# Performance work log

Measured on AMD Instinct MI355X. Metric: run time of the kernel, lower is better.

## Reference

```python
import jax, jax.numpy as jnp
import numpy as np

N = 400_000
D = 128          # voxel grid extent per axis
IN_CH = 64
OUT_CH = 64
BOUND = 2.0


def _build_neighbor_map(rng):
    # unique voxel coordinates in a D^3 grid
    flat = rng.choice(D ** 3, size=N, replace=False)
    lut = np.full(D ** 3, N, dtype=np.int32)   # sentinel N = no point
    lut[flat] = np.arange(N, dtype=np.int32)
    coords = np.stack(np.unravel_index(flat, (D, D, D)), axis=1).astype(np.int64)  # [N,3]
    offs = np.array([[i, j, k] for i in (-1, 0, 1) for j in (-1, 0, 1) for k in (-1, 0, 1)],
                    dtype=np.int64)  # [27,3]
    nbr = np.empty((27, N), dtype=np.int32)
    for k in range(27):
        nc = coords + offs[k]
        valid = np.all((nc >= 0) & (nc < D), axis=1)
        ncc = np.clip(nc, 0, D - 1)
        fl = (ncc[:, 0] * D + ncc[:, 1]) * D + ncc[:, 2]
        nbr[k] = np.where(valid, lut[fl], N)
    return jnp.asarray(nbr)


def setup_inputs() -> dict:
    key = jax.random.key(0)
    k1, k2, k3, k4 = jax.random.split(key, 4)
    rng = np.random.default_rng(0)
    nbr = _build_neighbor_map(rng)
    return {
        "x_feat": jax.random.normal(k1, (N, IN_CH), jnp.float32),
        "y_feat": jax.random.normal(k2, (N, IN_CH), jnp.float32),
        "w1": jax.random.normal(k3, (27, 2 * IN_CH, IN_CH), jnp.float32) * 0.05,
        "b1": jnp.zeros((IN_CH,), jnp.float32),
        "w2": jax.random.normal(k4, (27, IN_CH, OUT_CH), jnp.float32) * 0.05,
        "b2": jnp.zeros((OUT_CH,), jnp.float32),
        "nbr": nbr,
    }


def _sparse_conv(feats, w, b, nbr):
    # feats: [N, Cin]; w: [27, Cin, Cout]; nbr: [27, N] with sentinel N -> zero feature
    fpad = jnp.concatenate([feats, jnp.zeros((1, feats.shape[1]), feats.dtype)], axis=0)

    def step(acc, wk_nk):
        wk, nk = wk_nk
        return acc + fpad[nk] @ wk, None

    acc0 = jnp.zeros((feats.shape[0], w.shape[2]), feats.dtype)
    out, _ = jax.lax.scan(step, acc0, (w, nbr))
    return out + b


def reference(x_feat, y_feat, w1, b1, w2, b2, nbr):
    # ME.cat((x, y)): concat features on shared coordinate map
    feats = jnp.concatenate([x_feat, y_feat], axis=1)            # [N, 2*in_ch]
    h = _sparse_conv(feats, w1, b1, nbr)                         # ConvBlock 1
    h = jax.nn.relu(h)                                           # act='relu'
    h = _sparse_conv(h, w2, b2, nbr)                             # ConvBlock 2 (act=None)
    return jnp.clip(h, -BOUND, BOUND)                            # BoundFunction forward
```

## Files before the change

kernel.cpp:

```cpp
#include <hip/hip_runtime.h>
#include <stdint.h>


#define NPTS 400000
#define TAPS 27

typedef __attribute__((ext_vector_type(8))) _Float16 f16x8;
typedef __attribute__((ext_vector_type(4))) float f32x4;

#define MFMA16(a, b, c) __builtin_amdgcn_mfma_f32_16x16x32_f16(a, b, c, 0, 0, 0)

#define H16_BYTES ((size_t)(NPTS + 1) * 128)
#define W1T_SZ    ((size_t)TAPS * 64 * 128 * 2)
#define W2T_SZ    ((size_t)TAPS * 64 * 64 * 2)
#define W1T_OFF   (H16_BYTES)
#define W2T_OFF   (W1T_OFF + W1T_SZ)
#define XY16_OFF  (W2T_OFF + W2T_SZ)

__device__ inline void gload_lds16(const void* g, void* l) {
    __builtin_amdgcn_global_load_lds((const __attribute__((address_space(1))) void*)g,
                                     (__attribute__((address_space(3))) void*)l, 16, 0, 0);
}

__global__ __launch_bounds__(256) void prep_weights(
    const float* __restrict__ w1, const float* __restrict__ w2,
    _Float16* __restrict__ w1t, _Float16* __restrict__ w2t,
    _Float16* __restrict__ h16)
{
    const int gid = blockIdx.x * 256 + threadIdx.x;
    const int n1 = TAPS * 64 * 128;
    const int n2 = TAPS * 64 * 64;
    if (gid < n1) {
        const int tap = gid >> 13;
        const int q  = (gid & 8191) << 1;
        const int sb = q ^ (((q >> 8) & 15) << 4);
        const int col = sb >> 8, k = (sb & 255) >> 1;
        w1t[gid] = (_Float16)w1[((size_t)tap * 128 + k) * 64 + col];
    } else if (gid < n1 + n2) {
        const int g = gid - n1;
        const int tap = g >> 12;
        const int q  = (g & 4095) << 1;
        const int sb = q ^ (((q >> 7) & 7) << 4);
        const int col = sb >> 7, k = (sb & 127) >> 1;
        w2t[g] = (_Float16)w2[((size_t)tap * 64 + k) * 64 + col];
    } else if (gid < n1 + n2 + 64) {
        h16[(size_t)NPTS * 64 + (gid - n1 - n2)] = (_Float16)0.f;
    }
}

__global__ __launch_bounds__(256) void prep_xy16(
    const float* __restrict__ x, const float* __restrict__ y,
    _Float16* __restrict__ xy16)
{
    const int gid = blockIdx.x * 256 + threadIdx.x;
    if (gid >= (NPTS + 1) * 16) return;
    const int p = gid >> 4, seg = gid & 15;
    f32x4 v0 = {0.f, 0.f, 0.f, 0.f}, v1 = {0.f, 0.f, 0.f, 0.f};
    if (p < NPTS) {
        const float* s = (seg < 8) ? (x + (size_t)p * 64 + seg * 8)
                                   : (y + (size_t)p * 64 + (seg - 8) * 8);
        v0 = *(const f32x4*)s; v1 = *(const f32x4*)(s + 4);
    }
    _Float16 h[8];
#pragma unroll
    for (int j = 0; j < 4; ++j) { h[j] = (_Float16)v0[j]; h[4 + j] = (_Float16)v1[j]; }
    *(f16x8*)&xy16[(size_t)p * 128 + seg * 8] = *(f16x8*)h;
}

__global__ __launch_bounds__(256, 4) void conv1_kernel(
    const _Float16* __restrict__ xy16,
    const _Float16* __restrict__ w1t,
    const float* __restrict__ b1, const int* __restrict__ nbr,
    _Float16* __restrict__ h16)
{
    __shared__ char wsh[16384];

    const int tid = threadIdx.x;
    const int wv = tid >> 6, ln = tid & 63;
    const int g4 = ln >> 4, c = ln & 15;
    const int base = blockIdx.x * 128 + wv * 32;

    f32x4 acc[2][4];
    {
        float bv[4];
#pragma unroll
        for (int nf = 0; nf < 4; ++nf) bv[nf] = b1[16 * nf + c];
#pragma unroll
        for (int mi = 0; mi < 2; ++mi)
#pragma unroll
            for (int nf = 0; nf < 4; ++nf)
                acc[mi][nf] = (f32x4){bv[nf], bv[nf], bv[nf], bv[nf]};
    }

    int gi[2], gin[2];
    f16x8 aA[2], aB[2];

#define LOAD_IDX1(dst, tp) do { \
    _Pragma("unroll") for (int mi = 0; mi < 2; ++mi) \
        dst[mi] = nbr[(size_t)(tp) * NPTS + base + mi * 16 + c]; \
    } while (0)

#define GPRE1(dst, kf) do { \
    _Pragma("unroll") for (int mi = 0; mi < 2; ++mi) { \
        const char* row = (const char*)xy16 + (size_t)gi[mi] * 256; \
        dst[mi] = *(const f16x8*)(row + ((kf) << 6) + (g4 << 4)); \
    } } while (0)

#define COMP1(ab, kf) do { \
    _Pragma("unroll") for (int nf = 0; nf < 4; ++nf) { \
        const int addr = ((((16 * nf + c) << 8) + ((kf) << 6) + (g4 << 4))) ^ (c << 4); \
        const f16x8 wb = *(const f16x8*)&wsh[addr]; \
        _Pragma("unroll") for (int mi = 0; mi < 2; ++mi) \
            acc[mi][nf] = MFMA16(ab[mi], wb, acc[mi][nf]); \
    } } while (0)

#define STAGE_W1(tp) do { \
    const char* src = (const char*)w1t + (size_t)(tp) * 16384 + wv * 4096 + ln * 16; \
    _Pragma("unroll") for (int i = 0; i < 4; ++i) \
        gload_lds16(src + i * 1024, &wsh[wv * 4096 + i * 1024]); \
    } while (0)

    LOAD_IDX1(gi, 0);
    LOAD_IDX1(gin, 1);
    STAGE_W1(0);
    GPRE1(aA, 0);
    GPRE1(aB, 1);
    __syncthreads();

    for (int tap = 0; ; ++tap) {
        COMP1(aA, 0);
        GPRE1(aA, 2);
        COMP1(aB, 1);
        GPRE1(aB, 3);
        COMP1(aA, 2);
        const bool more = (tap + 1 < TAPS);
        if (more) {
#pragma unroll
            for (int mi = 0; mi < 2; ++mi) gi[mi] = gin[mi];
            const int tp2 = (tap + 2 < TAPS) ? tap + 2 : TAPS - 1;
            LOAD_IDX1(gin, tp2);
            GPRE1(aA, 0);
        }
        COMP1(aB, 3);
        if (!more) break;
        __syncthreads();
        STAGE_W1(tap + 1);
        GPRE1(aB, 1);
        __syncthreads();
    }

#pragma unroll
    for (int mi = 0; mi < 2; ++mi)
#pragma unroll
        for (int nf = 0; nf < 4; ++nf)
#pragma unroll
            for (int r = 0; r < 4; ++r) {
                const int pt = base + mi * 16 + (g4 << 2) + r;
                h16[(size_t)pt * 64 + 16 * nf + c] =
                    (_Float16)fmaxf(acc[mi][nf][r], 0.f);
            }
#undef LOAD_IDX1
#undef GPRE1
#undef COMP1
#undef STAGE_W1
}

__global__ __launch_bounds__(256, 4) void conv2_kernel(
    const _Float16* __restrict__ h16,
    const _Float16* __restrict__ w2t,
    const float* __restrict__ b2, const int* __restrict__ nbr,
    float* __restrict__ out)
{
    __shared__ char wsh[8192];

    const int tid = threadIdx.x;
    const int wv = tid >> 6, ln = tid & 63;
    const int g4 = ln >> 4, c = ln & 15;
    const int base = blockIdx.x * 128 + wv * 32;

    f32x4 acc[2][4];
    {
        float bv[4];
#pragma unroll
        for (int nf = 0; nf < 4; ++nf) bv[nf] = b2[16 * nf + c];
#pragma unroll
        for (int mi = 0; mi < 2; ++mi)
#pragma unroll
            for (int nf = 0; nf < 4; ++nf)
                acc[mi][nf] = (f32x4){bv[nf], bv[nf], bv[nf], bv[nf]};
    }

    int gi[2], gin[2];
    f16x8 aA[2], aB[2];

#define LOAD_IDX2(dst, tp) do { \
    _Pragma("unroll") for (int mi = 0; mi < 2; ++mi) \
        dst[mi] = nbr[(size_t)(tp) * NPTS + base + mi * 16 + c]; \
    } while (0)

#define GPRE2(dst, kf) do { \
    _Pragma("unroll") for (int mi = 0; mi < 2; ++mi) { \
        const char* row = (const char*)h16 + (size_t)gi[mi] * 128; \
        dst[mi] = *(const f16x8*)(row + ((kf) << 6) + (g4 << 4)); \
    } } while (0)

#define COMP2(ab, kf) do { \
    _Pragma("unroll") for (int nf = 0; nf < 4; ++nf) { \
        const int addr = ((((16 * nf + c) << 7) + ((kf) << 6) + (g4 << 4))) ^ ((c & 7) << 4); \
        const f16x8 wb = *(const f16x8*)&wsh[addr]; \
        _Pragma("unroll") for (int mi = 0; mi < 2; ++mi) \
            acc[mi][nf] = MFMA16(ab[mi], wb, acc[mi][nf]); \
    } } while (0)

#define STAGE_W2(tp) do { \
    const char* src = (const char*)w2t + (size_t)(tp) * 8192 + wv * 2048 + ln * 16; \
    _Pragma("unroll") for (int i = 0; i < 2; ++i) \
        gload_lds16(src + i * 1024, &wsh[wv * 2048 + i * 1024]); \
    } while (0)

    LOAD_IDX2(gi, 0);
    LOAD_IDX2(gin, 1);
    STAGE_W2(0);
    GPRE2(aA, 0);
    GPRE2(aB, 1);
    __syncthreads();

    for (int tap = 0; ; ++tap) {
        COMP2(aA, 0);
        const bool more = (tap + 1 < TAPS);
        if (more) {
#pragma unroll
            for (int mi = 0; mi < 2; ++mi) gi[mi] = gin[mi];
            const int tp2 = (tap + 2 < TAPS) ? tap + 2 : TAPS - 1;
            LOAD_IDX2(gin, tp2);
            GPRE2(aA, 0);
        }
        COMP2(aB, 1);
        if (!more) break;
        __syncthreads();
        STAGE_W2(tap + 1);
        GPRE2(aB, 1);
        __syncthreads();
    }

#pragma unroll
    for (int mi = 0; mi < 2; ++mi)
#pragma unroll
        for (int nf = 0; nf < 4; ++nf)
#pragma unroll
            for (int r = 0; r < 4; ++r) {
                const int pt = base + mi * 16 + (g4 << 2) + r;
                out[(size_t)pt * 64 + 16 * nf + c] =
                    fminf(fmaxf(acc[mi][nf][r], -2.f), 2.f);
            }
#undef LOAD_IDX2
#undef GPRE2
#undef COMP2
#undef STAGE_W2
}

extern "C" void kernel_launch(void* const* d_in, const int* in_sizes, int n_in,
                              void* d_out, int out_size, void* d_ws, size_t ws_size,
                              hipStream_t stream) {
    const float* x  = (const float*)d_in[0];
    const float* y  = (const float*)d_in[1];
    const float* w1 = (const float*)d_in[2];
    const float* b1 = (const float*)d_in[3];
    const float* w2 = (const float*)d_in[4];
    const float* b2 = (const float*)d_in[5];
    const int* nbr  = (const int*)d_in[6];
    float* out = (float*)d_out;

    char* ws = (char*)d_ws;
    _Float16* h16  = (_Float16*)ws;
    _Float16* w1t  = (_Float16*)(ws + W1T_OFF);
    _Float16* w2t  = (_Float16*)(ws + W2T_OFF);
    _Float16* xy16 = (_Float16*)(ws + XY16_OFF);

    const int prep_threads = TAPS * 64 * 128 + TAPS * 64 * 64 + 64;
    prep_weights<<<(prep_threads + 255) / 256, 256, 0, stream>>>(w1, w2, w1t, w2t, h16);

    const int pxy_threads = (NPTS + 1) * 16;
    prep_xy16<<<(pxy_threads + 255) / 256, 256, 0, stream>>>(x, y, xy16);

    conv1_kernel<<<NPTS / 128, 256, 0, stream>>>(xy16, w1t, b1, nbr, h16);
    conv2_kernel<<<NPTS / 128, 256, 0, stream>>>(h16, w2t, b2, nbr, out);
}
```

Baseline: 417.4 us.

## Prefetch whole next-tap gathered rows into double-buffered registers in both convs

```diff
diff --git a/kernel.cpp b/kernel.cpp
--- a/kernel.cpp
+++ b/kernel.cpp
@@ -93,17 +93,18 @@
     }
 
     int gi[2], gin[2];
-    f16x8 aA[2], aB[2];
+    f16x8 aE[2][4], aO[2][4];
 
 #define LOAD_IDX1(dst, tp) do { \
     _Pragma("unroll") for (int mi = 0; mi < 2; ++mi) \
         dst[mi] = nbr[(size_t)(tp) * NPTS + base + mi * 16 + c]; \
     } while (0)
 
-#define GPRE1(dst, kf) do { \
+#define GFULL1(dst) do { \
     _Pragma("unroll") for (int mi = 0; mi < 2; ++mi) { \
         const char* row = (const char*)xy16 + (size_t)gi[mi] * 256; \
-        dst[mi] = *(const f16x8*)(row + ((kf) << 6) + (g4 << 4)); \
+        _Pragma("unroll") for (int kf = 0; kf < 4; ++kf) \
+            dst[mi][kf] = *(const f16x8*)(row + (kf << 6) + (g4 << 4)); \
     } } while (0)
 
 #define COMP1(ab, kf) do { \
@@ -111,7 +112,7 @@
         const int addr = ((((16 * nf + c) << 8) + ((kf) << 6) + (g4 << 4))) ^ (c << 4); \
         const f16x8 wb = *(const f16x8*)&wsh[addr]; \
         _Pragma("unroll") for (int mi = 0; mi < 2; ++mi) \
-            acc[mi][nf] = MFMA16(ab[mi], wb, acc[mi][nf]); \
+            acc[mi][nf] = MFMA16(ab[mi][kf], wb, acc[mi][nf]); \
     } } while (0)
 
 #define STAGE_W1(tp) do { \
@@ -121,33 +122,39 @@
     } while (0)
 
     LOAD_IDX1(gi, 0);
+    GFULL1(aE);
     LOAD_IDX1(gin, 1);
     STAGE_W1(0);
-    GPRE1(aA, 0);
-    GPRE1(aB, 1);
     __syncthreads();
 
-    for (int tap = 0; ; ++tap) {
-        COMP1(aA, 0);
-        GPRE1(aA, 2);
-        COMP1(aB, 1);
-        GPRE1(aB, 3);
-        COMP1(aA, 2);
-        const bool more = (tap + 1 < TAPS);
-        if (more) {
-#pragma unroll
-            for (int mi = 0; mi < 2; ++mi) gi[mi] = gin[mi];
-            const int tp2 = (tap + 2 < TAPS) ? tap + 2 : TAPS - 1;
-            LOAD_IDX1(gin, tp2);
-            GPRE1(aA, 0);
-        }
-        COMP1(aB, 3);
-        if (!more) break;
-        __syncthreads();
-        STAGE_W1(tap + 1);
-        GPRE1(aB, 1);
-        __syncthreads();
-    }
+    for (int tp = 0; tp < 26; tp += 2) {
+#pragma unroll
+        for (int mi = 0; mi < 2; ++mi) gi[mi] = gin[mi];
+        LOAD_IDX1(gin, tp + 2);
+        GFULL1(aO);
+        COMP1(aE, 0);
+        COMP1(aE, 1);
+        COMP1(aE, 2);
+        COMP1(aE, 3);
+        __syncthreads();
+        STAGE_W1(tp + 1);
+        __syncthreads();
+#pragma unroll
+        for (int mi = 0; mi < 2; ++mi) gi[mi] = gin[mi];
+        LOAD_IDX1(gin, tp + 3 < TAPS ? tp + 3 : TAPS - 1);
+        GFULL1(aE);
+        COMP1(aO, 0);
+        COMP1(aO, 1);
+        COMP1(aO, 2);
+        COMP1(aO, 3);
+        __syncthreads();
+        STAGE_W1(tp + 2);
+        __syncthreads();
+    }
+    COMP1(aE, 0);
+    COMP1(aE, 1);
+    COMP1(aE, 2);
+    COMP1(aE, 3);
 
 #pragma unroll
     for (int mi = 0; mi < 2; ++mi)
@@ -160,7 +167,7 @@
                     (_Float16)fmaxf(acc[mi][nf][r], 0.f);
             }
 #undef LOAD_IDX1
-#undef GPRE1
+#undef GFULL1
 #undef COMP1
 #undef STAGE_W1
 }
@@ -191,17 +198,18 @@
     }
 
     int gi[2], gin[2];
-    f16x8 aA[2], aB[2];
+    f16x8 aE[2][2], aO[2][2];
 
 #define LOAD_IDX2(dst, tp) do { \
     _Pragma("unroll") for (int mi = 0; mi < 2; ++mi) \
         dst[mi] = nbr[(size_t)(tp) * NPTS + base + mi * 16 + c]; \
     } while (0)
 
-#define GPRE2(dst, kf) do { \
+#define GFULL2(dst) do { \
     _Pragma("unroll") for (int mi = 0; mi < 2; ++mi) { \
         const char* row = (const char*)h16 + (size_t)gi[mi] * 128; \
-        dst[mi] = *(const f16x8*)(row + ((kf) << 6) + (g4 << 4)); \
+        _Pragma("unroll") for (int kf = 0; kf < 2; ++kf) \
+            dst[mi][kf] = *(const f16x8*)(row + (kf << 6) + (g4 << 4)); \
     } } while (0)
 
 #define COMP2(ab, kf) do { \
@@ -209,7 +217,7 @@
         const int addr = ((((16 * nf + c) << 7) + ((kf) << 6) + (g4 << 4))) ^ ((c & 7) << 4); \
         const f16x8 wb = *(const f16x8*)&wsh[addr]; \
         _Pragma("unroll") for (int mi = 0; mi < 2; ++mi) \
-            acc[mi][nf] = MFMA16(ab[mi], wb, acc[mi][nf]); \
+            acc[mi][nf] = MFMA16(ab[mi][kf], wb, acc[mi][nf]); \
     } } while (0)
 
 #define STAGE_W2(tp) do { \
@@ -219,29 +227,33 @@
     } while (0)
 
     LOAD_IDX2(gi, 0);
+    GFULL2(aE);
     LOAD_IDX2(gin, 1);
     STAGE_W2(0);
-    GPRE2(aA, 0);
-    GPRE2(aB, 1);
     __syncthreads();
 
-    for (int tap = 0; ; ++tap) {
-        COMP2(aA, 0);
-        const bool more = (tap + 1 < TAPS);
-        if (more) {
-#pragma unroll
-            for (int mi = 0; mi < 2; ++mi) gi[mi] = gin[mi];
-            const int tp2 = (tap + 2 < TAPS) ? tap + 2 : TAPS - 1;
-            LOAD_IDX2(gin, tp2);
-            GPRE2(aA, 0);
-        }
-        COMP2(aB, 1);
-        if (!more) break;
-        __syncthreads();
-        STAGE_W2(tap + 1);
-        GPRE2(aB, 1);
-        __syncthreads();
-    }
+    for (int tp = 0; tp < 26; tp += 2) {
+#pragma unroll
+        for (int mi = 0; mi < 2; ++mi) gi[mi] = gin[mi];
+        LOAD_IDX2(gin, tp + 2);
+        GFULL2(aO);
+        COMP2(aE, 0);
+        COMP2(aE, 1);
+        __syncthreads();
+        STAGE_W2(tp + 1);
+        __syncthreads();
+#pragma unroll
+        for (int mi = 0; mi < 2; ++mi) gi[mi] = gin[mi];
+        LOAD_IDX2(gin, tp + 3 < TAPS ? tp + 3 : TAPS - 1);
+        GFULL2(aE);
+        COMP2(aO, 0);
+        COMP2(aO, 1);
+        __syncthreads();
+        STAGE_W2(tp + 2);
+        __syncthreads();
+    }
+    COMP2(aE, 0);
+    COMP2(aE, 1);
 
 #pragma unroll
     for (int mi = 0; mi < 2; ++mi)
@@ -254,7 +266,7 @@
                     fminf(fmaxf(acc[mi][nf][r], -2.f), 2.f);
             }
 #undef LOAD_IDX2
-#undef GPRE2
+#undef GFULL2
 #undef COMP2
 #undef STAGE_W2
 }
```

Result: slower. 489.3 us (+17.2%).
